# Kernel optimization log

Measured on AMD Instinct MI355X. Metric: run time of the kernel, lower is better.

## Reference

```python
import jax, jax.numpy as jnp
import numpy as np

B, S, E, H = 4, 2048, 1024, 16
D = E // H
FF = 4096
LN_EPS = 1e-3  # Keras LayerNormalization default epsilon


def _layernorm(x, g, b):
    mu = jnp.mean(x, axis=-1, keepdims=True)
    var = jnp.mean(jnp.square(x - mu), axis=-1, keepdims=True)
    return (x - mu) * jax.lax.rsqrt(var + LN_EPS) * g + b


def setup_inputs() -> dict:
    key = jax.random.key(0)
    ks = jax.random.split(key, 16)
    s = lambda fan_in: 1.0 / np.sqrt(fan_in)
    inp = {
        "x": jax.random.normal(ks[0], (B, S, E), jnp.float32),
        "mask": jnp.ones((B, S), dtype=bool),
        "Wq": jax.random.normal(ks[1], (E, E), jnp.float32) * s(E),
        "bq": jnp.zeros((E,), jnp.float32),
        "Wk": jax.random.normal(ks[2], (E, E), jnp.float32) * s(E),
        "bk": jnp.zeros((E,), jnp.float32),
        "Wv": jax.random.normal(ks[3], (E, E), jnp.float32) * s(E),
        "bv": jnp.zeros((E,), jnp.float32),
        "Wo": jax.random.normal(ks[4], (E, E), jnp.float32) * s(E),
        "bo": jnp.zeros((E,), jnp.float32),
        "W1": jax.random.normal(ks[5], (E, FF), jnp.float32) * s(E),
        "b1": jnp.zeros((FF,), jnp.float32),
        "W2": jax.random.normal(ks[6], (FF, E), jnp.float32) * s(FF),
        "b2": jnp.zeros((E,), jnp.float32),
        "ln1_g": jnp.ones((E,), jnp.float32),
        "ln1_b": jnp.zeros((E,), jnp.float32),
        "ln2_g": jnp.ones((E,), jnp.float32),
        "ln2_b": jnp.zeros((E,), jnp.float32),
    }
    return inp


def reference(x, mask, Wq, bq, Wk, bk, Wv, bv, Wo, bo, W1, b1, W2, b2,
              ln1_g, ln1_b, ln2_g, ln2_b):
    # --- multi-head self attention (manual matmul + softmax + matmul) ---
    def heads(t):  # [B,S,E] -> [B,H,S,D]
        return t.reshape(B, S, H, D).transpose(0, 2, 1, 3)

    q = heads(x @ Wq + bq)
    k = heads(x @ Wk + bk)
    v = heads(x @ Wv + bv)

    scores = jnp.einsum("bhqd,bhkd->bhqk", q, k) / jnp.sqrt(jnp.float32(D))
    m = mask.astype(jnp.float32)[:, None, None, :]  # [B,1,1,S]
    scores = scores + (-1e9) * (1.0 - m)
    weights = jax.nn.softmax(scores, axis=-1)
    attn = jnp.einsum("bhqk,bhkd->bhqd", weights, v)
    attn = attn.transpose(0, 2, 1, 3).reshape(B, S, E)
    attn = attn @ Wo + bo

    # residual + layernorm (dropout is identity: training=False)
    h = _layernorm(x + attn, ln1_g, ln1_b)

    # --- FFN ---
    ff = jax.nn.relu(h @ W1 + b1) @ W2 + b2
    out = _layernorm(h + ff, ln2_g, ln2_b)
    return out
```

## Files before the change

### kernel.cpp

```cpp
#include <hip/hip_runtime.h>
#include <stdint.h>
#include <stddef.h>

#define Bn 4
#define Sn 2048
#define En 1024
#define Hn 16
#define Dn 64
#define FFn 4096
#define Mn (Bn*Sn)

typedef __bf16 bf16_t;
typedef __bf16 bf16x8 __attribute__((ext_vector_type(8)));
typedef __bf16 bf16x4 __attribute__((ext_vector_type(4)));
typedef float  f32x4  __attribute__((ext_vector_type(4)));
typedef float  f32x16 __attribute__((ext_vector_type(16)));

#define AS1 __attribute__((address_space(1)))
#define AS3 __attribute__((address_space(3)))

#define EXP2F(x) __builtin_amdgcn_exp2f(x)

static __device__ __forceinline__ void gload_lds16(const bf16_t* g, void* l) {
    __builtin_amdgcn_global_load_lds((const AS1 void*)g, (AS3 void*)l, 16, 0, 0);
}

__global__ __launch_bounds__(256)
void cvt_bf16(const float* __restrict__ xin, bf16_t* __restrict__ xout, int n)
{
    int i = (blockIdx.x * 256 + threadIdx.x) * 4;
    if (i >= n) return;
    float4 f = *(const float4*)(xin + i);
    bf16x4 o;
    o[0] = (bf16_t)f.x; o[1] = (bf16_t)f.y; o[2] = (bf16_t)f.z; o[3] = (bf16_t)f.w;
    *(bf16x4*)(xout + i) = o;
}

__global__ __launch_bounds__(256)
void transp_bf16(const float* __restrict__ W, bf16_t* __restrict__ WT, int R, int C)
{
    __shared__ float t[32][33];
    const int tx = threadIdx.x & 31, ty = threadIdx.x >> 5;
    const int c0 = blockIdx.x * 32, r0 = blockIdx.y * 32;
    #pragma unroll
    for (int i = ty; i < 32; i += 8)
        t[i][tx] = W[(size_t)(r0 + i) * C + c0 + tx];
    __syncthreads();
    #pragma unroll
    for (int i = ty; i < 32; i += 8)
        WT[(size_t)(c0 + i) * R + r0 + tx] = (bf16_t)t[tx][i];
}

__global__ __launch_bounds__(256)
void concat_bias(const float* __restrict__ a, const float* __restrict__ b,
                 const float* __restrict__ c, float* __restrict__ o)
{
    int i = blockIdx.x * 256 + threadIdx.x;
    o[i] = (i < 1024) ? a[i] : ((i < 2048) ? b[i - 1024] : c[i - 2048]);
}

template<int MODE>
__global__ __launch_bounds__(512)
void gemm3r(const bf16_t* __restrict__ A, const bf16_t* __restrict__ BT,
            const float* __restrict__ bias,
            float* __restrict__ Cf, bf16_t* __restrict__ Cb,
            int Ndim, int Kdim)
{
    extern __shared__ char smem[];
    bf16_t* lA = (bf16_t*)smem;
    bf16_t* lB = (bf16_t*)(smem + 3 * 256 * 64 * 2);

    const int tid = threadIdx.x, lane = tid & 63;
    const int w = tid >> 6, wm = w >> 1, wn = w & 1;
    const int bm = blockIdx.y, bn = blockIdx.x;

    const int srow = tid >> 3;
    const int ssl  = tid & 7;
    const int swz  = (ssl ^ (srow & 7)) * 8;
    const bf16_t* Ab = A  + (size_t)(bm * 256 + srow) * Kdim + swz;
    const bf16_t* Bb = BT + (size_t)(bn * 128 + srow) * Kdim + swz;
    const int ldst = srow * 64 + ssl * 8;

    const int ntiles = Kdim >> 6;

    f32x4 acc[4][4] = {};

    const int arow0 = (wm * 64 + (lane & 15)) * 64;
    const int brow0 = (wn * 64 + (lane & 15)) * 64;
    const int g0 = (((lane >> 4)    ) ^ (lane & 7)) * 8;
    const int g1 = ((4 + (lane >> 4)) ^ (lane & 7)) * 8;

    #define STAGE3(r, kt) do {                                                  \
        bf16_t* a_ = lA + (r) * (256 * 64) + ldst;                              \
        bf16_t* b_ = lB + (r) * (128 * 64) + ldst;                              \
        const bf16_t* ga_ = Ab + (kt) * 64;                                     \
        const bf16_t* gb_ = Bb + (kt) * 64;                                     \
        gload_lds16(ga_,                          a_);                          \
        gload_lds16(ga_ + (size_t)64  * Kdim,     a_ + 64 * 64);                \
        gload_lds16(ga_ + (size_t)128 * Kdim,     a_ + 128 * 64);               \
        gload_lds16(ga_ + (size_t)192 * Kdim,     a_ + 192 * 64);               \
        gload_lds16(gb_,                          b_);                          \
        gload_lds16(gb_ + (size_t)64  * Kdim,     b_ + 64 * 64);                \
    } while (0)

    STAGE3(0, 0);
    STAGE3(1, 1);

    for (int t = 0; t < ntiles; ++t) {
        if (t + 2 < ntiles) asm volatile("s_waitcnt vmcnt(6)" ::: "memory");
        else                asm volatile("s_waitcnt vmcnt(0)" ::: "memory");
        __builtin_amdgcn_s_barrier();
        __builtin_amdgcn_sched_barrier(0);
        if (t + 2 < ntiles) STAGE3((t + 2) % 3, t + 2);

        const bf16_t* pa = lA + (t % 3) * (256 * 64) + arow0;
        const bf16_t* pb = lB + (t % 3) * (128 * 64) + brow0;
        bf16x8 aF[4][2], bF[4][2];
        #pragma unroll
        for (int m = 0; m < 4; ++m) {
            aF[m][0] = *(const bf16x8*)(pa + m * 16 * 64 + g0);
            aF[m][1] = *(const bf16x8*)(pa + m * 16 * 64 + g1);
        }
        #pragma unroll
        for (int n = 0; n < 4; ++n) {
            bF[n][0] = *(const bf16x8*)(pb + n * 16 * 64 + g0);
            bF[n][1] = *(const bf16x8*)(pb + n * 16 * 64 + g1);
        }
        __builtin_amdgcn_s_setprio(1);
        #pragma unroll
        for (int m = 0; m < 4; ++m)
            #pragma unroll
            for (int n = 0; n < 4; ++n) {
                acc[m][n] = __builtin_amdgcn_mfma_f32_16x16x32_bf16(
                                aF[m][0], bF[n][0], acc[m][n], 0, 0, 0);
                acc[m][n] = __builtin_amdgcn_mfma_f32_16x16x32_bf16(
                                aF[m][1], bF[n][1], acc[m][n], 0, 0, 0);
            }
        __builtin_amdgcn_s_setprio(0);
    }
    #undef STAGE3

    const size_t ME = (size_t)Mn * En;
    const int fc = lane & 15;
    const int fr = (lane >> 4) * 4;
    #pragma unroll
    for (int n = 0; n < 4; ++n) {
        const int gcol = bn * 128 + wn * 64 + n * 16 + fc;
        const float bv = bias[gcol];
        #pragma unroll
        for (int m = 0; m < 4; ++m) {
            const int growb = bm * 256 + wm * 64 + m * 16 + fr;
            #pragma unroll
            for (int j = 0; j < 4; ++j) {
                const int grow = growb + j;
                float v = acc[m][n][j] + bv;
                if constexpr (MODE == 0) {
                    Cf[(size_t)grow * Ndim + gcol] = v;
                } else if constexpr (MODE == 2) {
                    Cb[(size_t)grow * Ndim + gcol] = (bf16_t)fmaxf(v, 0.f);
                } else {
                    const int id = gcol >> 10;
                    const int c1 = gcol & 1023;
                    const int b = grow >> 11, s = grow & 2047;
                    const int h = c1 >> 6,    d = c1 & 63;
                    if (id < 2)
                        Cb[(size_t)id * ME + (((size_t)(b * 16 + h) << 11) + s) * 64 + d] = (bf16_t)v;
                    else
                        Cb[2 * ME + (((size_t)(b * 16 + h) * 64 + d) << 11) + s] = (bf16_t)v;
                }
            }
        }
    }
}

static __device__ __forceinline__ uint32_t pack2_bf16(float a, float b) {
    union { bf16_t h[2]; uint32_t u; } v;
    v.h[0] = (bf16_t)a; v.h[1] = (bf16_t)b;
    return v.u;
}

#define PSWAP(a,b) asm volatile("v_permlane32_swap_b32 %0, %1" : "+v"(a), "+v"(b))

__global__ __launch_bounds__(256)
void attn_kernel(const bf16_t* __restrict__ qh, const bf16_t* __restrict__ kh,
                 const bf16_t* __restrict__ vt, bf16_t* __restrict__ attnF)
{
    __shared__ bf16_t lk[2][64 * 64];
    __shared__ bf16_t lv[2][64 * 64];

    const int tid = threadIdx.x, lane = tid & 63, w = tid >> 6;
    const int hi = lane >> 5, q = lane & 31;

    const int fid = blockIdx.x;
    const int xcd = fid & 7, idx = fid >> 3;
    const int bh  = xcd + 8 * (idx & 7);
    const int qb  = idx >> 3;
    const int q0  = qb * 128 + w * 32;

    const bf16_t* Kbase = kh + (size_t)bh * Sn * 64;
    const bf16_t* Vbase = vt + (size_t)bh * 64 * Sn;

    const float qsc = 0.125f * 1.4426950408889634f;
    bf16x8 qf[4];
    {
        const bf16_t* Qp = qh + ((size_t)bh * Sn + q0 + q) * 64 + hi * 8;
        #pragma unroll
        for (int kc = 0; kc < 4; ++kc) {
            bf16x8 r = *(const bf16x8*)(Qp + kc * 16);
            #pragma unroll
            for (int j = 0; j < 8; ++j) qf[kc][j] = (bf16_t)(qsc * (float)r[j]);
        }
    }

    const int sr = lane >> 3, ssl = lane & 7;
    const int gsoff = ((ssl ^ sr) * 8);

    f32x16 o0 = {}, o1 = {};
    float m_run = -1e30f, l_run = 0.f;

    #pragma unroll
    for (int c = 0; c < 2; ++c) {
        const int g = 2 * w + c, row = g * 8 + sr;
        gload_lds16(Kbase + (size_t)row * 64 + gsoff, &lk[0][g * 8 * 64]);
        gload_lds16(Vbase + (size_t)row * Sn + gsoff, &lv[0][g * 8 * 64]);
    }
    __syncthreads();

    int cur = 0;
    for (int it = 0; it < Sn / 64; ++it) {
        if (it + 1 < Sn / 64) {
            const int nkb = (it + 1) * 64;
            #pragma unroll
            for (int c = 0; c < 2; ++c) {
                const int g = 2 * w + c, row = g * 8 + sr;
                gload_lds16(Kbase + (size_t)(nkb + row) * 64 + gsoff, &lk[cur ^ 1][g * 8 * 64]);
                gload_lds16(Vbase + (size_t)row * Sn + nkb + gsoff,   &lv[cur ^ 1][g * 8 * 64]);
            }
        }

        f32x16 sc0 = {}, sc1 = {};
        __builtin_amdgcn_s_setprio(1);
        #pragma unroll
        for (int kc = 0; kc < 4; ++kc) {
            const int sl = ((2 * kc + hi) ^ (q & 7)) * 8;
            bf16x8 k0 = *(const bf16x8*)(&lk[cur][q * 64 + sl]);
            bf16x8 k1 = *(const bf16x8*)(&lk[cur][(32 + q) * 64 + sl]);
            sc0 = __builtin_amdgcn_mfma_f32_32x32x16_bf16(k0, qf[kc], sc0, 0, 0, 0);
            sc1 = __builtin_amdgcn_mfma_f32_32x32x16_bf16(k1, qf[kc], sc1, 0, 0, 0);
        }
        __builtin_amdgcn_s_setprio(0);

        float mx = -1e30f;
        #pragma unroll
        for (int r = 0; r < 16; ++r) mx = fmaxf(mx, fmaxf(sc0[r], sc1[r]));
        mx = fmaxf(mx, __shfl_xor(mx, 32));
        const float mnew = fmaxf(m_run, mx);
        const float corr = EXP2F(m_run - mnew);
        float p0[16], p1[16];
        float rs = 0.f;
        #pragma unroll
        for (int r = 0; r < 16; ++r) {
            p0[r] = EXP2F(sc0[r] - mnew);
            p1[r] = EXP2F(sc1[r] - mnew);
            rs += p0[r] + p1[r];
        }
        rs += __shfl_xor(rs, 32);
        l_run = l_run * corr + rs;
        m_run = mnew;
        #pragma unroll
        for (int r = 0; r < 16; ++r) { o0[r] *= corr; o1[r] *= corr; }

        bf16x8 pb[4];
        {
            union { uint32_t u[4]; bf16x8 v; } fr;
            #pragma unroll
            for (int f = 0; f < 2; ++f) {
                uint32_t u0 = pack2_bf16(p0[8*f+0], p0[8*f+1]);
                uint32_t u1 = pack2_bf16(p0[8*f+2], p0[8*f+3]);
                uint32_t u2 = pack2_bf16(p0[8*f+4], p0[8*f+5]);
                uint32_t u3 = pack2_bf16(p0[8*f+6], p0[8*f+7]);
                PSWAP(u0, u2); PSWAP(u1, u3);
                fr.u[0] = u0; fr.u[1] = u1; fr.u[2] = u2; fr.u[3] = u3;
                pb[f] = fr.v;
            }
            #pragma unroll
            for (int f = 0; f < 2; ++f) {
                uint32_t u0 = pack2_bf16(p1[8*f+0], p1[8*f+1]);
                uint32_t u1 = pack2_bf16(p1[8*f+2], p1[8*f+3]);
                uint32_t u2 = pack2_bf16(p1[8*f+4], p1[8*f+5]);
                uint32_t u3 = pack2_bf16(p1[8*f+6], p1[8*f+7]);
                PSWAP(u0, u2); PSWAP(u1, u3);
                fr.u[0] = u0; fr.u[1] = u1; fr.u[2] = u2; fr.u[3] = u3;
                pb[2 + f] = fr.v;
            }
        }

        __builtin_amdgcn_s_setprio(1);
        #pragma unroll
        for (int sk = 0; sk < 4; ++sk) {
            const int sl = ((2 * sk + hi) ^ (q & 7)) * 8;
            bf16x8 v0 = *(const bf16x8*)(&lv[cur][q * 64 + sl]);
            bf16x8 v1 = *(const bf16x8*)(&lv[cur][(32 + q) * 64 + sl]);
            o0 = __builtin_amdgcn_mfma_f32_32x32x16_bf16(v0, pb[sk], o0, 0, 0, 0);
            o1 = __builtin_amdgcn_mfma_f32_32x32x16_bf16(v1, pb[sk], o1, 0, 0, 0);
        }
        __builtin_amdgcn_s_setprio(0);

        __syncthreads();
        cur ^= 1;
    }

    const float linv = 1.f / l_run;
    const int b = bh >> 4, h = bh & 15;
    bf16_t* dst = attnF + ((size_t)b * Sn + q0 + q) * En + h * 64;
    #pragma unroll
    for (int grp = 0; grp < 4; ++grp) {
        bf16x4 w0, w1;
        #pragma unroll
        for (int j = 0; j < 4; ++j) {
            w0[j] = (bf16_t)(o0[4 * grp + j] * linv);
            w1[j] = (bf16_t)(o1[4 * grp + j] * linv);
        }
        *(bf16x4*)(dst + grp * 8 + 4 * hi)      = w0;
        *(bf16x4*)(dst + 32 + grp * 8 + 4 * hi) = w1;
    }
}

__global__ __launch_bounds__(256)
void ln_kernel(const float* __restrict__ res, const float* __restrict__ proj,
               const float* __restrict__ gamma, const float* __restrict__ beta,
               float* __restrict__ outf, bf16_t* __restrict__ outb)
{
    const int row = blockIdx.x;
    const int tid = threadIdx.x;
    const size_t base = (size_t)row * En + tid * 4;
    float v[4];
    #pragma unroll
    for (int i = 0; i < 4; ++i)
        v[i] = res[base + i] + proj[base + i];

    float s = 0.f, ss = 0.f;
    #pragma unroll
    for (int i = 0; i < 4; ++i) { s += v[i]; ss += v[i] * v[i]; }
    #pragma unroll
    for (int off = 1; off < 64; off <<= 1) {
        s  += __shfl_xor(s, off);
        ss += __shfl_xor(ss, off);
    }
    __shared__ float sm[8];
    const int wv = tid >> 6;
    if ((tid & 63) == 0) { sm[wv] = s; sm[4 + wv] = ss; }
    __syncthreads();
    s  = sm[0] + sm[1] + sm[2] + sm[3];
    ss = sm[4] + sm[5] + sm[6] + sm[7];
    const float mu   = s * (1.f / En);
    const float var  = ss * (1.f / En) - mu * mu;
    const float rstd = rsqrtf(var + 1e-3f);
    #pragma unroll
    for (int i = 0; i < 4; ++i) {
        const int c = tid * 4 + i;
        const float o = (v[i] - mu) * rstd * gamma[c] + beta[c];
        if (outf) outf[base + i] = o;
        if (outb) outb[base + i] = (bf16_t)o;
    }
}

extern "C" void kernel_launch(void* const* d_in, const int* in_sizes, int n_in,
                              void* d_out, int out_size, void* d_ws, size_t ws_size,
                              hipStream_t stream)
{
    (void)in_sizes; (void)n_in; (void)out_size; (void)ws_size;
    const float* x   = (const float*)d_in[0];
    const float* Wq  = (const float*)d_in[2];
    const float* bq  = (const float*)d_in[3];
    const float* Wk  = (const float*)d_in[4];
    const float* bk  = (const float*)d_in[5];
    const float* Wv  = (const float*)d_in[6];
    const float* bv  = (const float*)d_in[7];
    const float* Wo  = (const float*)d_in[8];
    const float* bo  = (const float*)d_in[9];
    const float* W1  = (const float*)d_in[10];
    const float* b1  = (const float*)d_in[11];
    const float* W2  = (const float*)d_in[12];
    const float* b2  = (const float*)d_in[13];
    const float* g1  = (const float*)d_in[14];
    const float* be1 = (const float*)d_in[15];
    const float* g2  = (const float*)d_in[16];
    const float* be2 = (const float*)d_in[17];
    float* out = (float*)d_out;

    char* p = (char*)d_ws;
    const size_t ME = (size_t)Mn * En;
    bf16_t* xb    = (bf16_t*)p;  p += ME * 2;
    bf16_t* WqT   = (bf16_t*)p;  p += (size_t)En * En * 2;
    bf16_t* WkT   = (bf16_t*)p;  p += (size_t)En * En * 2;
    bf16_t* WvT   = (bf16_t*)p;  p += (size_t)En * En * 2;
    bf16_t* WoT   = (bf16_t*)p;  p += (size_t)En * En * 2;
    bf16_t* W1T   = (bf16_t*)p;  p += (size_t)FFn * En * 2;
    bf16_t* W2T   = (bf16_t*)p;  p += (size_t)En * FFn * 2;
    bf16_t* qh    = (bf16_t*)p;  p += ME * 2;
    bf16_t* kh    = (bf16_t*)p;  p += ME * 2;
    bf16_t* vt    = (bf16_t*)p;  p += ME * 2;
    bf16_t* attnF = (bf16_t*)p;  p += ME * 2;
    bf16_t* hb    = (bf16_t*)p;  p += ME * 2;
    bf16_t* ff    = (bf16_t*)p;  p += (size_t)Mn * FFn * 2;
    float*  bqkv  = (float*)p;   p += 3072 * 4;
    float*  hf32  = (float*)qh;

    const dim3 blk(256);
    const int GEMM_LDS = (3 * 256 * 64 + 3 * 128 * 64) * 2;

    static bool attr_done = false;
    if (!attr_done) {
        hipFuncSetAttribute((const void*)gemm3r<0>, hipFuncAttributeMaxDynamicSharedMemorySize, GEMM_LDS);
        hipFuncSetAttribute((const void*)gemm3r<2>, hipFuncAttributeMaxDynamicSharedMemorySize, GEMM_LDS);
        hipFuncSetAttribute((const void*)gemm3r<5>, hipFuncAttributeMaxDynamicSharedMemorySize, GEMM_LDS);
        attr_done = true;
    }

    cvt_bf16<<<dim3(Mn * En / 1024), blk, 0, stream>>>(x, xb, Mn * En);
    transp_bf16<<<dim3(32, 32),  blk, 0, stream>>>(Wq, WqT, En, En);
    transp_bf16<<<dim3(32, 32),  blk, 0, stream>>>(Wk, WkT, En, En);
    transp_bf16<<<dim3(32, 32),  blk, 0, stream>>>(Wv, WvT, En, En);
    transp_bf16<<<dim3(32, 32),  blk, 0, stream>>>(Wo, WoT, En, En);
    transp_bf16<<<dim3(128, 32), blk, 0, stream>>>(W1, W1T, En, FFn);
    transp_bf16<<<dim3(32, 128), blk, 0, stream>>>(W2, W2T, FFn, En);
    concat_bias<<<dim3(12), blk, 0, stream>>>(bq, bk, bv, bqkv);

    gemm3r<5><<<dim3(24, 32), dim3(512), GEMM_LDS, stream>>>(xb, WqT, bqkv, nullptr, qh, 3072, En);

    attn_kernel<<<dim3(1024), blk, 0, stream>>>(qh, kh, vt, attnF);

    gemm3r<0><<<dim3(8, 32), dim3(512), GEMM_LDS, stream>>>(attnF, WoT, bo, out, nullptr, En, En);
    ln_kernel<<<dim3(Mn), blk, 0, stream>>>(x, out, g1, be1, hf32, hb);

    gemm3r<2><<<dim3(32, 32), dim3(512), GEMM_LDS, stream>>>(hb, W1T, b1, nullptr, ff, FFn, En);
    gemm3r<0><<<dim3(8, 32), dim3(512), GEMM_LDS, stream>>>(ff, W2T, b2, out, nullptr, En, FFn);

    ln_kernel<<<dim3(Mn), blk, 0, stream>>>(hf32, out, g2, be2, out, nullptr);
}
```

Measured before the change: 510.6 us.

## Use 256x256 GEMM tiles, split-K for W2, lazy softmax rescaling in attention

```diff
diff --git a/kernel.cpp b/kernel.cpp
--- a/kernel.cpp
+++ b/kernel.cpp
@@ -61,95 +61,98 @@
 
 template<int MODE>
 __global__ __launch_bounds__(512)
-void gemm3r(const bf16_t* __restrict__ A, const bf16_t* __restrict__ BT,
-            const float* __restrict__ bias,
-            float* __restrict__ Cf, bf16_t* __restrict__ Cb,
-            int Ndim, int Kdim)
+void gemm256(const bf16_t* __restrict__ A, const bf16_t* __restrict__ BT,
+             const float* __restrict__ bias,
+             float* __restrict__ Cf, float* __restrict__ Cf2,
+             bf16_t* __restrict__ Cb,
+             int Ndim, int kext, int lda, int ldb)
 {
     extern __shared__ char smem[];
     bf16_t* lA = (bf16_t*)smem;
-    bf16_t* lB = (bf16_t*)(smem + 3 * 256 * 64 * 2);
+    bf16_t* lB = (bf16_t*)(smem + 2 * 256 * 64 * 2);
 
     const int tid = threadIdx.x, lane = tid & 63;
-    const int w = tid >> 6, wm = w >> 1, wn = w & 1;
-    const int bm = blockIdx.y, bn = blockIdx.x;
+    const int w = tid >> 6, wm = w >> 2, wn = w & 3;
+    const int bm = blockIdx.y, bn = blockIdx.x, bz = blockIdx.z;
 
     const int srow = tid >> 3;
     const int ssl  = tid & 7;
     const int swz  = (ssl ^ (srow & 7)) * 8;
-    const bf16_t* Ab = A  + (size_t)(bm * 256 + srow) * Kdim + swz;
-    const bf16_t* Bb = BT + (size_t)(bn * 128 + srow) * Kdim + swz;
+    const bf16_t* Ab = A  + (size_t)bz * kext + (size_t)(bm * 256 + srow) * lda + swz;
+    const bf16_t* Bb = BT + (size_t)bz * kext + (size_t)(bn * 256 + srow) * ldb + swz;
     const int ldst = srow * 64 + ssl * 8;
 
-    const int ntiles = Kdim >> 6;
-
-    f32x4 acc[4][4] = {};
-
-    const int arow0 = (wm * 64 + (lane & 15)) * 64;
-    const int brow0 = (wn * 64 + (lane & 15)) * 64;
-    const int g0 = (((lane >> 4)    ) ^ (lane & 7)) * 8;
-    const int g1 = ((4 + (lane >> 4)) ^ (lane & 7)) * 8;
-
-    #define STAGE3(r, kt) do {                                                  \
-        bf16_t* a_ = lA + (r) * (256 * 64) + ldst;                              \
-        bf16_t* b_ = lB + (r) * (128 * 64) + ldst;                              \
-        const bf16_t* ga_ = Ab + (kt) * 64;                                     \
-        const bf16_t* gb_ = Bb + (kt) * 64;                                     \
-        gload_lds16(ga_,                          a_);                          \
-        gload_lds16(ga_ + (size_t)64  * Kdim,     a_ + 64 * 64);                \
-        gload_lds16(ga_ + (size_t)128 * Kdim,     a_ + 128 * 64);               \
-        gload_lds16(ga_ + (size_t)192 * Kdim,     a_ + 192 * 64);               \
-        gload_lds16(gb_,                          b_);                          \
-        gload_lds16(gb_ + (size_t)64  * Kdim,     b_ + 64 * 64);                \
+    const int ntiles = kext >> 6;
+
+    f32x4 acc[8][4] = {};
+
+    const int arow0 = (wm * 128 + (lane & 15)) * 64;
+    const int brow0 = (wn * 64  + (lane & 15)) * 64;
+    const int gg0 = (((lane >> 4)    ) ^ (lane & 7)) * 8;
+    const int gg1 = ((4 + (lane >> 4)) ^ (lane & 7)) * 8;
+
+    #define STAGE(slot, kt) do {                                               \
+        bf16_t* a_ = lA + (slot) * (256 * 64) + ldst;                          \
+        bf16_t* b_ = lB + (slot) * (256 * 64) + ldst;                          \
+        const bf16_t* ga_ = Ab + (size_t)(kt) * 64;                            \
+        const bf16_t* gb_ = Bb + (size_t)(kt) * 64;                            \
+        gload_lds16(ga_,                        a_);                           \
+        gload_lds16(ga_ + (size_t)64  * lda,    a_ + 64 * 64);                 \
+        gload_lds16(ga_ + (size_t)128 * lda,    a_ + 128 * 64);                \
+        gload_lds16(ga_ + (size_t)192 * lda,    a_ + 192 * 64);                \
+        gload_lds16(gb_,                        b_);                           \
+        gload_lds16(gb_ + (size_t)64  * ldb,    b_ + 64 * 64);                 \
+        gload_lds16(gb_ + (size_t)128 * ldb,    b_ + 128 * 64);                \
+        gload_lds16(gb_ + (size_t)192 * ldb,    b_ + 192 * 64);                \
     } while (0)
 
-    STAGE3(0, 0);
-    STAGE3(1, 1);
+    STAGE(0, 0);
+    STAGE(1, 1);
 
     for (int t = 0; t < ntiles; ++t) {
-        if (t + 2 < ntiles) asm volatile("s_waitcnt vmcnt(6)" ::: "memory");
+        if (t + 1 < ntiles) asm volatile("s_waitcnt vmcnt(8)" ::: "memory");
         else                asm volatile("s_waitcnt vmcnt(0)" ::: "memory");
         __builtin_amdgcn_s_barrier();
         __builtin_amdgcn_sched_barrier(0);
-        if (t + 2 < ntiles) STAGE3((t + 2) % 3, t + 2);
-
-        const bf16_t* pa = lA + (t % 3) * (256 * 64) + arow0;
-        const bf16_t* pb = lB + (t % 3) * (128 * 64) + brow0;
-        bf16x8 aF[4][2], bF[4][2];
-        #pragma unroll
-        for (int m = 0; m < 4; ++m) {
-            aF[m][0] = *(const bf16x8*)(pa + m * 16 * 64 + g0);
-            aF[m][1] = *(const bf16x8*)(pa + m * 16 * 64 + g1);
-        }
-        #pragma unroll
-        for (int n = 0; n < 4; ++n) {
-            bF[n][0] = *(const bf16x8*)(pb + n * 16 * 64 + g0);
-            bF[n][1] = *(const bf16x8*)(pb + n * 16 * 64 + g1);
-        }
+
+        const bf16_t* pa = lA + (t & 1) * (256 * 64) + arow0;
+        const bf16_t* pb = lB + (t & 1) * (256 * 64) + brow0;
+
         __builtin_amdgcn_s_setprio(1);
         #pragma unroll
-        for (int m = 0; m < 4; ++m)
-            #pragma unroll
-            for (int n = 0; n < 4; ++n) {
-                acc[m][n] = __builtin_amdgcn_mfma_f32_16x16x32_bf16(
-                                aF[m][0], bF[n][0], acc[m][n], 0, 0, 0);
-                acc[m][n] = __builtin_amdgcn_mfma_f32_16x16x32_bf16(
-                                aF[m][1], bF[n][1], acc[m][n], 0, 0, 0);
+        for (int kh = 0; kh < 2; ++kh) {
+            const int g = kh ? gg1 : gg0;
+            bf16x8 bF[4];
+            #pragma unroll
+            for (int n = 0; n < 4; ++n)
+                bF[n] = *(const bf16x8*)(pb + n * 16 * 64 + g);
+            #pragma unroll
+            for (int m = 0; m < 8; ++m) {
+                bf16x8 aF = *(const bf16x8*)(pa + m * 16 * 64 + g);
+                #pragma unroll
+                for (int n = 0; n < 4; ++n)
+                    acc[m][n] = __builtin_amdgcn_mfma_f32_16x16x32_bf16(
+                                    aF, bF[n], acc[m][n], 0, 0, 0);
             }
+        }
         __builtin_amdgcn_s_setprio(0);
-    }
-    #undef STAGE3
+
+        __builtin_amdgcn_s_barrier();
+        __builtin_amdgcn_sched_barrier(0);
+        if (t + 2 < ntiles) STAGE(t & 1, t + 2);
+    }
+    #undef STAGE
 
     const size_t ME = (size_t)Mn * En;
     const int fc = lane & 15;
     const int fr = (lane >> 4) * 4;
     #pragma unroll
     for (int n = 0; n < 4; ++n) {
-        const int gcol = bn * 128 + wn * 64 + n * 16 + fc;
-        const float bv = bias[gcol];
-        #pragma unroll
-        for (int m = 0; m < 4; ++m) {
-            const int growb = bm * 256 + wm * 64 + m * 16 + fr;
+        const int gcol = bn * 256 + wn * 64 + n * 16 + fc;
+        const float bv = (MODE == 6) ? 0.f : bias[gcol];
+        #pragma unroll
+        for (int m = 0; m < 8; ++m) {
+            const int growb = bm * 256 + wm * 128 + m * 16 + fr;
             #pragma unroll
             for (int j = 0; j < 4; ++j) {
                 const int grow = growb + j;
@@ -158,7 +161,7 @@
                     Cf[(size_t)grow * Ndim + gcol] = v;
                 } else if constexpr (MODE == 2) {
                     Cb[(size_t)grow * Ndim + gcol] = (bf16_t)fmaxf(v, 0.f);
-                } else {
+                } else if constexpr (MODE == 5) {
                     const int id = gcol >> 10;
                     const int c1 = gcol & 1023;
                     const int b = grow >> 11, s = grow & 2047;
@@ -167,6 +170,9 @@
                         Cb[(size_t)id * ME + (((size_t)(b * 16 + h) << 11) + s) * 64 + d] = (bf16_t)v;
                     else
                         Cb[2 * ME + (((size_t)(b * 16 + h) * 64 + d) << 11) + s] = (bf16_t)v;
+                } else {
+                    float* dst = bz ? Cf2 : Cf;
+                    dst[(size_t)grow * Ndim + gcol] = v;
                 }
             }
         }
@@ -254,21 +260,25 @@
         #pragma unroll
         for (int r = 0; r < 16; ++r) mx = fmaxf(mx, fmaxf(sc0[r], sc1[r]));
         mx = fmaxf(mx, __shfl_xor(mx, 32));
-        const float mnew = fmaxf(m_run, mx);
-        const float corr = EXP2F(m_run - mnew);
+
+        if (!__all(mx - m_run <= 8.0f)) {
+            const float mnew = fmaxf(m_run, mx);
+            const float corr = EXP2F(m_run - mnew);
+            l_run *= corr;
+            m_run = mnew;
+            #pragma unroll
+            for (int r = 0; r < 16; ++r) { o0[r] *= corr; o1[r] *= corr; }
+        }
         float p0[16], p1[16];
         float rs = 0.f;
         #pragma unroll
         for (int r = 0; r < 16; ++r) {
-            p0[r] = EXP2F(sc0[r] - mnew);
-            p1[r] = EXP2F(sc1[r] - mnew);
+            p0[r] = EXP2F(sc0[r] - m_run);
+            p1[r] = EXP2F(sc1[r] - m_run);
             rs += p0[r] + p1[r];
         }
         rs += __shfl_xor(rs, 32);
-        l_run = l_run * corr + rs;
-        m_run = mnew;
-        #pragma unroll
-        for (int r = 0; r < 16; ++r) { o0[r] *= corr; o1[r] *= corr; }
+        l_run += rs;
 
         bf16x8 pb[4];
         {
@@ -362,6 +372,44 @@
         const float o = (v[i] - mu) * rstd * gamma[c] + beta[c];
         if (outf) outf[base + i] = o;
         if (outb) outb[base + i] = (bf16_t)o;
+    }
+}
+
+__global__ __launch_bounds__(256)
+void ln2_kernel(const float* __restrict__ res, const float* __restrict__ p1,
+                const float* __restrict__ p2, const float* __restrict__ bias2,
+                const float* __restrict__ gamma, const float* __restrict__ beta,
+                float* __restrict__ outf)
+{
+    const int row = blockIdx.x;
+    const int tid = threadIdx.x;
+    const size_t base = (size_t)row * En + tid * 4;
+    float v[4];
+    #pragma unroll
+    for (int i = 0; i < 4; ++i)
+        v[i] = res[base + i] + p1[base + i] + p2[base + i] + bias2[tid * 4 + i];
+
+    float s = 0.f, ss = 0.f;
+    #pragma unroll
+    for (int i = 0; i < 4; ++i) { s += v[i]; ss += v[i] * v[i]; }
+    #pragma unroll
+    for (int off = 1; off < 64; off <<= 1) {
+        s  += __shfl_xor(s, off);
+        ss += __shfl_xor(ss, off);
+    }
+    __shared__ float sm[8];
+    const int wv = tid >> 6;
+    if ((tid & 63) == 0) { sm[wv] = s; sm[4 + wv] = ss; }
+    __syncthreads();
+    s  = sm[0] + sm[1] + sm[2] + sm[3];
+    ss = sm[4] + sm[5] + sm[6] + sm[7];
+    const float mu   = s * (1.f / En);
+    const float var  = ss * (1.f / En) - mu * mu;
+    const float rstd = rsqrtf(var + 1e-3f);
+    #pragma unroll
+    for (int i = 0; i < 4; ++i) {
+        const int c = tid * 4 + i;
+        outf[base + i] = (v[i] - mu) * rstd * gamma[c] + beta[c];
     }
 }
 
@@ -406,15 +454,17 @@
     bf16_t* ff    = (bf16_t*)p;  p += (size_t)Mn * FFn * 2;
     float*  bqkv  = (float*)p;   p += 3072 * 4;
     float*  hf32  = (float*)qh;
+    float*  part2 = (float*)attnF;
 
     const dim3 blk(256);
-    const int GEMM_LDS = (3 * 256 * 64 + 3 * 128 * 64) * 2;
+    const int G_LDS = 2 * (256 * 64 + 256 * 64) * 2;
 
     static bool attr_done = false;
     if (!attr_done) {
-        hipFuncSetAttribute((const void*)gemm3r<0>, hipFuncAttributeMaxDynamicSharedMemorySize, GEMM_LDS);
-        hipFuncSetAttribute((const void*)gemm3r<2>, hipFuncAttributeMaxDynamicSharedMemorySize, GEMM_LDS);
-        hipFuncSetAttribute((const void*)gemm3r<5>, hipFuncAttributeMaxDynamicSharedMemorySize, GEMM_LDS);
+        hipFuncSetAttribute((const void*)gemm256<0>, hipFuncAttributeMaxDynamicSharedMemorySize, G_LDS);
+        hipFuncSetAttribute((const void*)gemm256<2>, hipFuncAttributeMaxDynamicSharedMemorySize, G_LDS);
+        hipFuncSetAttribute((const void*)gemm256<5>, hipFuncAttributeMaxDynamicSharedMemorySize, G_LDS);
+        hipFuncSetAttribute((const void*)gemm256<6>, hipFuncAttributeMaxDynamicSharedMemorySize, G_LDS);
         attr_done = true;
     }
 
@@ -427,15 +477,20 @@
     transp_bf16<<<dim3(32, 128), blk, 0, stream>>>(W2, W2T, FFn, En);
     concat_bias<<<dim3(12), blk, 0, stream>>>(bq, bk, bv, bqkv);
 
-    gemm3r<5><<<dim3(24, 32), dim3(512), GEMM_LDS, stream>>>(xb, WqT, bqkv, nullptr, qh, 3072, En);
+    gemm256<5><<<dim3(12, 32), dim3(512), G_LDS, stream>>>(
+        xb, WqT, bqkv, nullptr, nullptr, qh, 3072, En, En, En);
 
     attn_kernel<<<dim3(1024), blk, 0, stream>>>(qh, kh, vt, attnF);
 
-    gemm3r<0><<<dim3(8, 32), dim3(512), GEMM_LDS, stream>>>(attnF, WoT, bo, out, nullptr, En, En);
+    gemm256<0><<<dim3(4, 32), dim3(512), G_LDS, stream>>>(
+        attnF, WoT, bo, out, nullptr, nullptr, En, En, En, En);
     ln_kernel<<<dim3(Mn), blk, 0, stream>>>(x, out, g1, be1, hf32, hb);
 
-    gemm3r<2><<<dim3(32, 32), dim3(512), GEMM_LDS, stream>>>(hb, W1T, b1, nullptr, ff, FFn, En);
-    gemm3r<0><<<dim3(8, 32), dim3(512), GEMM_LDS, stream>>>(ff, W2T, b2, out, nullptr, En, FFn);
-
-    ln_kernel<<<dim3(Mn), blk, 0, stream>>>(hf32, out, g2, be2, out, nullptr);
-}
+    gemm256<2><<<dim3(16, 32), dim3(512), G_LDS, stream>>>(
+        hb, W1T, b1, nullptr, nullptr, ff, FFn, En, En, En);
+
+    gemm256<6><<<dim3(4, 32, 2), dim3(512), G_LDS, stream>>>(
+        ff, W2T, nullptr, out, part2, nullptr, En, FFn / 2, FFn, FFn);
+
+    ln2_kernel<<<dim3(Mn), blk, 0, stream>>>(hf32, out, part2, b2, g2, be2, out);
+}
```

Measured after the change: 488.8 us. 1.04x faster.
